# Kernel optimization log

Measured on AMD Instinct MI355X. Metric: run time of the kernel, lower is better.

## Reference

```python
import jax, jax.numpy as jnp
import numpy as np

BATCH = 64
N_NODES = 1000
SEQ = 12
FEAT = 4          # in_features_per_node // N_history
IN_CH = 48        # in_features_per_node, also GAT out_channels
HEADS = 2
OUT_FEAT = 2      # out_features_per_node
H1, H2 = 256, 128
N_TOTAL = BATCH * N_NODES
E = 1024000


def setup_inputs() -> dict:
    key = jax.random.key(0)
    ks = jax.random.split(key, 16)
    s = 0.05
    return {
        "x": jax.random.normal(ks[0], (N_TOTAL, IN_CH), jnp.float32),
        "edge_index": jax.random.randint(ks[1], (2, E), 0, N_TOTAL, jnp.int64),
        "W_gat": jax.random.normal(ks[2], (IN_CH, HEADS * IN_CH), jnp.float32) * s,
        "att_src": jax.random.normal(ks[3], (HEADS, IN_CH), jnp.float32) * s,
        "att_dst": jax.random.normal(ks[4], (HEADS, IN_CH), jnp.float32) * s,
        "gat_bias": jax.random.normal(ks[5], (IN_CH,), jnp.float32) * s,
        "W_ih1": jax.random.normal(ks[6], (4 * H1, N_NODES * FEAT), jnp.float32) * s,
        "W_hh1": jax.random.normal(ks[7], (4 * H1, H1), jnp.float32) * s,
        "b1": jnp.zeros((4 * H1,), jnp.float32),
        "W_ih2": jax.random.normal(ks[8], (4 * H2, H1), jnp.float32) * s,
        "W_hh2": jax.random.normal(ks[9], (4 * H2, H2), jnp.float32) * s,
        "b2": jnp.zeros((4 * H2,), jnp.float32),
        "W_out": jax.random.normal(ks[10], (N_NODES * OUT_FEAT, H2), jnp.float32) * s,
        "b_out": jnp.zeros((N_NODES * OUT_FEAT,), jnp.float32),
    }


def _gat_conv(x, edge_index, W_gat, att_src, att_dst, gat_bias):
    """PyG GATConv, heads=HEADS, concat=False (mean over heads), add_self_loops=True."""
    N = x.shape[0]
    h = (x @ W_gat).reshape(N, HEADS, IN_CH)              # [N,H,C]
    a_src = jnp.einsum('nhc,hc->nh', h, att_src)          # [N,H]
    a_dst = jnp.einsum('nhc,hc->nh', h, att_dst)
    loops = jnp.arange(N, dtype=edge_index.dtype)
    src = jnp.concatenate([edge_index[0], loops])         # [E+N]
    dst = jnp.concatenate([edge_index[1], loops])
    e = jax.nn.leaky_relu(a_src[src] + a_dst[dst], 0.2)   # [E+N,H]
    # segment-softmax over incoming edges of each destination node
    m = jnp.full((N, HEADS), -jnp.inf, e.dtype).at[dst].max(e)
    w = jnp.exp(e - m[dst])
    denom = jax.ops.segment_sum(w, dst, num_segments=N)
    alpha = w / (denom[dst] + 1e-16)                      # [E+N,H]
    msg = h[src] * alpha[:, :, None]                      # [E+N,H,C]
    out = jax.ops.segment_sum(msg, dst, num_segments=N)   # [N,H,C]
    return out.mean(axis=1) + gat_bias                    # [N,C]


def _lstm(x_seq, W_ih, W_hh, b):
    """Single-layer LSTM, PyTorch gate order (i,f,g,o). x_seq: [T,B,D]."""
    Hs = W_hh.shape[1]
    B = x_seq.shape[1]
    xw = jnp.einsum('tbd,gd->tbg', x_seq, W_ih) + b       # precompute input proj

    def step(carry, xt):
        h, c = carry
        g = xt + h @ W_hh.T
        i, f, gg, o = jnp.split(g, 4, axis=-1)
        i, f, o = jax.nn.sigmoid(i), jax.nn.sigmoid(f), jax.nn.sigmoid(o)
        c = f * c + i * jnp.tanh(gg)
        h = o * jnp.tanh(c)
        return (h, c), h

    h0 = jnp.zeros((B, Hs), x_seq.dtype)
    _, ys = jax.lax.scan(step, (h0, h0), xw)
    return ys                                             # [T,B,Hs]


def reference(x, edge_index, W_gat, att_src, att_dst, gat_bias,
              W_ih1, W_hh1, b1, W_ih2, W_hh2, b2, W_out, b_out):
    g = _gat_conv(x, edge_index, W_gat, att_src, att_dst, gat_bias)  # [N_total, 48]
    # (B, N_nodes, SEQ, FEAT) -> movedim(2,0) -> (SEQ, B, N_nodes*FEAT)
    g = g.reshape(BATCH, N_NODES, SEQ, FEAT)
    g = jnp.moveaxis(g, 2, 0).reshape(SEQ, BATCH, N_NODES * FEAT)
    y = _lstm(g, W_ih1, W_hh1, b1)
    y = _lstm(y, W_ih2, W_hh2, b2)
    last = y[-1]                                          # [B, H2]
    out = last @ W_out.T + b_out                          # [B, N_nodes*OUT_FEAT]
    return out.reshape(BATCH * N_NODES, OUT_FEAT)
```

## Files before the change

kernel.cpp:

```cpp
#include <hip/hip_runtime.h>
#include <hip/hip_fp16.h>
#include <math.h>

#define NTOT   64000
#define NNODE  1000
#define NBATCH 64
#define NSEQ   12
#define NE     1024000

typedef _Float16 half8 __attribute__((ext_vector_type(8)));
typedef float f32x4 __attribute__((ext_vector_type(4)));

__device__ __forceinline__ float lrelu(float x){ return x > 0.f ? x : 0.2f*x; }
__device__ __forceinline__ float sigmoidf_(float x){ return 1.f/(1.f+__expf(-x)); }

__global__ void __launch_bounds__(256) k_gat_h(const float* __restrict__ x, const float* __restrict__ Wg,
                       const float* __restrict__ att_s, const float* __restrict__ att_d,
                       __half* __restrict__ hfeat, float* __restrict__ asrc, float* __restrict__ adst){
  __shared__ __align__(16) float Ws[48*96];
  __shared__ float as_s[96], ad_s[96];
  for (int i = threadIdx.x; i < 48*96; i += 256) Ws[i] = Wg[i];
  if (threadIdx.x < 96){ as_s[threadIdx.x] = att_s[threadIdx.x]; ad_s[threadIdx.x] = att_d[threadIdx.x]; }
  __syncthreads();
  int n = blockIdx.x * 256 + threadIdx.x;
  if (n >= NTOT) return;
  float xr[48];
  const float4* xv = (const float4*)(x + (size_t)n*48);
  #pragma unroll
  for (int q = 0; q < 12; ++q){ float4 v = xv[q]; xr[q*4]=v.x; xr[q*4+1]=v.y; xr[q*4+2]=v.z; xr[q*4+3]=v.w; }
  float a0=0.f,a1=0.f,d0=0.f,d1=0.f;
  __half* hrow = hfeat + (size_t)n*96;
  float prev = 0.f;
  for (int j = 0; j < 96; ++j){
    float acc = 0.f;
    #pragma unroll
    for (int k = 0; k < 48; ++k) acc += xr[k]*Ws[k*96+j];
    if (j & 1){
      __half2 p; p.x = __float2half(prev); p.y = __float2half(acc);
      *(__half2*)(hrow + j - 1) = p;
    } else prev = acc;
    if (j < 48){ a0 += acc*as_s[j]; d0 += acc*ad_s[j]; }
    else       { a1 += acc*as_s[j]; d1 += acc*ad_s[j]; }
  }
  asrc[n*2]=a0; asrc[n*2+1]=a1; adst[n*2]=d0; adst[n*2+1]=d1;
}

__global__ void k_count(const int* __restrict__ ei, int* __restrict__ cnt){
  int e = blockIdx.x*256 + threadIdx.x;
  if (e < NE) atomicAdd(&cnt[ei[NE + e]], 1);
}

__global__ void __launch_bounds__(256) k_scan1(const int* __restrict__ cnt, int* __restrict__ wsum){
  int w = (blockIdx.x*256 + threadIdx.x) >> 6;
  int lane = threadIdx.x & 63;
  int v = cnt[w*64 + lane];
  int t = v;
  #pragma unroll
  for (int d = 1; d < 64; d <<= 1) t += __shfl_xor(t, d);
  if (lane == 0) wsum[w] = t;
}

__global__ void __launch_bounds__(1024) k_scan2(int* __restrict__ wsum){
  __shared__ int tmp[1024];
  int k = threadIdx.x;
  int v = (k < 1000) ? wsum[k] : 0;
  tmp[k] = v; __syncthreads();
  for (int d = 1; d < 1024; d <<= 1){
    int t = (k >= d) ? tmp[k-d] : 0;
    __syncthreads();
    tmp[k] += t;
    __syncthreads();
  }
  if (k < 1000) wsum[k] = tmp[k] - v;
}

__global__ void __launch_bounds__(256) k_scan3(const int* __restrict__ cnt, const int* __restrict__ wpre,
                                               int* __restrict__ offs, int* __restrict__ cursor){
  int w = (blockIdx.x*256 + threadIdx.x) >> 6;
  int lane = threadIdx.x & 63;
  int i = w*64 + lane;
  int v = cnt[i];
  int x = v;
  #pragma unroll
  for (int d = 1; d < 64; d <<= 1){
    int t = __shfl_up(x, d);
    if (lane >= d) x += t;
  }
  int excl = wpre[w] + x - v;
  offs[i] = excl; cursor[i] = excl;
  if (i == NTOT-1) offs[NTOT] = excl + v;
}

__global__ void k_scatter(const int* __restrict__ ei, int* __restrict__ cursor, int* __restrict__ csr){
  int e = blockIdx.x*256 + threadIdx.x;
  if (e < NE){
    int d = ei[NE + e], s = ei[e];
    int pos = atomicAdd(&cursor[d], 1);
    csr[pos] = s;
  }
}

__global__ void __launch_bounds__(256) k_node(const __half* __restrict__ hf, const float* __restrict__ asrc,
                      const float* __restrict__ adst, const int* __restrict__ offs,
                      const int* __restrict__ csr, const float* __restrict__ bias,
                      _Float16* __restrict__ xseqh){
  __shared__ float gsh[4][96];
  int wv = threadIdx.x >> 6, lane = threadIdx.x & 63;
  int n = blockIdx.x*4 + wv;
  int off = offs[n], deg = offs[n+1] - off;
  const float2* as2 = (const float2*)asrc;
  float2 adn = ((const float2*)adst)[n];
  float2 asn = as2[n];
  float es0 = __expf(lrelu(asn.x + adn.x));
  float es1 = __expf(lrelu(asn.y + adn.y));
  int cl = (lane < 48) ? lane : lane - 48;
  bool h0 = (lane < 24);
  float wself = h0 ? es0 : es1;
  float ssum = wself;
  float2 acc;
  {
    __half2 r2 = *(const __half2*)(hf + (size_t)n*96 + 2*cl);
    float2 r = __half22float2(r2);
    acc.x = r.x*wself; acc.y = r.y*wself;
  }
  int i = 0;
  for (; i + 4 <= deg; i += 4){
    int ss[4];
    #pragma unroll
    for (int j = 0; j < 4; ++j) ss[j] = csr[off+i+j];
    float2 aa[4];
    #pragma unroll
    for (int j = 0; j < 4; ++j) aa[j] = as2[ss[j]];
    __half2 rr[4];
    #pragma unroll
    for (int j = 0; j < 4; ++j) rr[j] = *(const __half2*)(hf + (size_t)ss[j]*96 + 2*cl);
    #pragma unroll
    for (int j = 0; j < 4; ++j){
      float w0 = __expf(lrelu(aa[j].x + adn.x));
      float w1 = __expf(lrelu(aa[j].y + adn.y));
      float ws = h0 ? w0 : w1;
      float2 r = __half22float2(rr[j]);
      acc.x += r.x*ws; acc.y += r.y*ws;
      ssum += ws;
    }
  }
  for (; i < deg; ++i){
    int s = csr[off+i];
    float2 a = as2[s];
    __half2 r2 = *(const __half2*)(hf + (size_t)s*96 + 2*cl);
    float w0 = __expf(lrelu(a.x + adn.x));
    float w1 = __expf(lrelu(a.y + adn.y));
    float ws = h0 ? w0 : w1;
    float2 r = __half22float2(r2);
    acc.x += r.x*ws; acc.y += r.y*ws;
    ssum += ws;
  }
  float inv = 1.f/(ssum + 1e-16f);
  if (lane < 48){ gsh[wv][2*cl] = acc.x*inv; gsh[wv][2*cl+1] = acc.y*inv; }
  __syncthreads();
  if (lane < 48){
    float g = 0.5f*(gsh[wv][lane] + gsh[wv][48+lane]) + bias[lane];
    int b = n / 1000, node = n - b*1000;
    int t = lane >> 2, f = lane & 3;
    xseqh[((size_t)(t*64 + b))*4000 + node*4 + f] = (_Float16)g;
  }
}

__global__ void __launch_bounds__(256) k_prep(const float* __restrict__ Wih1,
                    const float* __restrict__ Whh1, const float* __restrict__ Wih2,
                    const float* __restrict__ Whh2,
                    _Float16* __restrict__ Bh, __half* __restrict__ dst){
  int blk = blockIdx.x;
  if (blk < 4000){
    int i = blk*256 + threadIdx.x;
    float4 v = *(const float4*)(Wih1 + (size_t)i*4);
    union { _Float16 h[4]; uint2 u; } o;
    o.h[0] = (_Float16)v.x; o.h[1] = (_Float16)v.y;
    o.h[2] = (_Float16)v.z; o.h[3] = (_Float16)v.w;
    *(uint2*)(Bh + (size_t)i*4) = o.u;
    return;
  }
  int i = (blk-4000)*256 + threadIdx.x;
  if (i < 262144){ int q = i>>10, r = i&1023; dst[i] = __float2half(Whh1[r*256+q]); return; }
  i -= 262144;
  if (i < 131072){ int q = i>>9, r = i&511; dst[262144+i] = __float2half(Wih2[r*256+q]); return; }
  i -= 131072;
  if (i < 65536){ int q = i>>9, r = i&511; dst[393216+i] = __float2half(Whh2[(size_t)r*128+q]); }
}

__global__ void __launch_bounds__(256) k_gemm1h(const _Float16* __restrict__ A,
                        const _Float16* __restrict__ B, const float* __restrict__ b1,
                        float* __restrict__ xw1){
  __shared__ _Float16 As[64*40];
  __shared__ _Float16 Bs[64*40];
  int tid = threadIdx.x;
  int w = tid >> 6, l = tid & 63;
  int m0 = blockIdx.x*64, n0 = blockIdx.y*64;
  int fr = l & 15, fk = (l >> 4)*8;
  f32x4 acc0 = {0.f,0.f,0.f,0.f}, acc1 = acc0, acc2 = acc0, acc3 = acc0;
  int ra = tid >> 2, ca = (tid & 3)*8;
  const _Float16* Ap = A + (size_t)(m0+ra)*4000 + ca;
  const _Float16* Bp = B + (size_t)(n0+ra)*4000 + ca;
  _Float16* Asw = &As[ra*40 + ca];
  _Float16* Bsw = &Bs[ra*40 + ca];
  half8 pa = *(const half8*)Ap;
  half8 pb = *(const half8*)Bp;
  for (int k0 = 0; k0 < 4000; k0 += 32){
    *(half8*)Asw = pa;
    *(half8*)Bsw = pb;
    __syncthreads();
    if (k0 + 32 < 4000){
      pa = *(const half8*)(Ap + k0 + 32);
      pb = *(const half8*)(Bp + k0 + 32);
    }
    half8 af  = *(const half8*)&As[(w*16 + fr)*40 + fk];
    half8 bf0 = *(const half8*)&Bs[( 0 + fr)*40 + fk];
    half8 bf1 = *(const half8*)&Bs[(16 + fr)*40 + fk];
    half8 bf2 = *(const half8*)&Bs[(32 + fr)*40 + fk];
    half8 bf3 = *(const half8*)&Bs[(48 + fr)*40 + fk];
    acc0 = __builtin_amdgcn_mfma_f32_16x16x32_f16(af, bf0, acc0, 0, 0, 0);
    acc1 = __builtin_amdgcn_mfma_f32_16x16x32_f16(af, bf1, acc1, 0, 0, 0);
    acc2 = __builtin_amdgcn_mfma_f32_16x16x32_f16(af, bf2, acc2, 0, 0, 0);
    acc3 = __builtin_amdgcn_mfma_f32_16x16x32_f16(af, bf3, acc3, 0, 0, 0);
    __syncthreads();
  }
  int mrow = m0 + w*16 + (l >> 4)*4;
  int ncol = n0 + (l & 15);
  float bb0 = b1[ncol], bb1 = b1[ncol+16], bb2 = b1[ncol+32], bb3 = b1[ncol+48];
  #pragma unroll
  for (int r = 0; r < 4; ++r){
    float* cp = xw1 + (size_t)(mrow + r)*1024 + ncol;
    cp[0]  = acc0[r] + bb0;
    cp[16] = acc1[r] + bb1;
    cp[32] = acc2[r] + bb2;
    cp[48] = acc3[r] + bb3;
  }
}

__device__ __forceinline__ void mac8(float* acc, uint4 wv, float hq){
  const __half2* hp = (const __half2*)&wv;
  float2 f0 = __half22float2(hp[0]);
  float2 f1 = __half22float2(hp[1]);
  float2 f2 = __half22float2(hp[2]);
  float2 f3 = __half22float2(hp[3]);
  acc[0] += f0.x*hq; acc[1] += f0.y*hq;
  acc[2] += f1.x*hq; acc[3] += f1.y*hq;
  acc[4] += f2.x*hq; acc[5] += f2.y*hq;
  acc[6] += f3.x*hq; acc[7] += f3.y*hq;
}

__global__ void __launch_bounds__(1024) k_lstm(
    const float* __restrict__ xw1, const __half* __restrict__ W1,
    const __half* __restrict__ W2i, const __half* __restrict__ W2h,
    const float* __restrict__ b2, float* __restrict__ h2o){
  __shared__ float h1s[256];
  __shared__ float h2s[128];
  __shared__ __align__(16) float pA[8192];
  __shared__ __align__(16) float pB[8192];
  int t = threadIdx.x;
  int b = blockIdx.x;
  int kk1 = t >> 7, c1c = (t & 127) * 8;
  int kk2 = t >> 6, c2c = (t & 63) * 8;
  int u2 = t - 256;
  float cc1 = 0.f, cc2 = 0.f;
  float b2r[4] = {0.f,0.f,0.f,0.f};
  if (t >= 256 && t < 384){
    #pragma unroll
    for (int gi = 0; gi < 4; ++gi) b2r[gi] = b2[gi*128 + u2];
  }
  if (t < 256) h1s[t] = 0.f;
  if (t < 128) h2s[t] = 0.f;
  __syncthreads();

  for (int k = 0; k <= NSEQ; ++k){
    float xg[4] = {0.f,0.f,0.f,0.f};
    if (k < NSEQ && t < 256){
      const float* xr = xw1 + ((size_t)k*64 + b)*1024 + t;
      #pragma unroll
      for (int gi = 0; gi < 4; ++gi) xg[gi] = xr[gi*256];
    }
    if (k < NSEQ){
      float acc[8] = {0,0,0,0,0,0,0,0};
      const __half* wp = W1 + (size_t)(kk1*32)*1024 + c1c;
      const float* hb = &h1s[kk1*32];
      #pragma unroll 4
      for (int q = 0; q < 32; ++q)
        mac8(acc, *(const uint4*)(wp + (size_t)q*1024), hb[q]);
      float4 w0; w0.x=acc[0]; w0.y=acc[1]; w0.z=acc[2]; w0.w=acc[3];
      float4 w1; w1.x=acc[4]; w1.y=acc[5]; w1.z=acc[6]; w1.w=acc[7];
      *(float4*)&pA[kk1*1024 + c1c]     = w0;
      *(float4*)&pA[kk1*1024 + c1c + 4] = w1;
    }
    if (k >= 1){
      float acch[8] = {0,0,0,0,0,0,0,0};
      const __half* wi = W2i + (size_t)(kk2*16)*512 + c2c;
      const float* hb1 = &h1s[kk2*16];
      #pragma unroll 4
      for (int q = 0; q < 16; ++q)
        mac8(acch, *(const uint4*)(wi + (size_t)q*512), hb1[q]);
      const __half* wh = W2h + (size_t)(kk2*8)*512 + c2c;
      const float* hb2 = &h2s[kk2*8];
      #pragma unroll 4
      for (int q = 0; q < 8; ++q)
        mac8(acch, *(const uint4*)(wh + (size_t)q*512), hb2[q]);
      float4 w0; w0.x=acch[0]; w0.y=acch[1]; w0.z=acch[2]; w0.w=acch[3];
      float4 w1; w1.x=acch[4]; w1.y=acch[5]; w1.z=acch[6]; w1.w=acch[7];
      *(float4*)&pB[kk2*512 + c2c]     = w0;
      *(float4*)&pB[kk2*512 + c2c + 4] = w1;
    }
    __syncthreads();
    if (k < NSEQ && t < 256){
      float g[4];
      #pragma unroll
      for (int gi = 0; gi < 4; ++gi){
        float s = xg[gi];
        #pragma unroll
        for (int kk = 0; kk < 8; ++kk) s += pA[kk*1024 + gi*256 + t];
        g[gi] = s;
      }
      float i_ = sigmoidf_(g[0]);
      float f_ = sigmoidf_(g[1]);
      float gg = tanhf(g[2]);
      float o_ = sigmoidf_(g[3]);
      cc1 = f_*cc1 + i_*gg;
      h1s[t] = o_*tanhf(cc1);
    }
    if (k >= 1 && t >= 256 && t < 384){
      float g[4];
      #pragma unroll
      for (int gi = 0; gi < 4; ++gi){
        float s = b2r[gi];
        #pragma unroll
        for (int kk = 0; kk < 16; ++kk) s += pB[kk*512 + gi*128 + u2];
        g[gi] = s;
      }
      float i_ = sigmoidf_(g[0]);
      float f_ = sigmoidf_(g[1]);
      float gg = tanhf(g[2]);
      float o_ = sigmoidf_(g[3]);
      cc2 = f_*cc2 + i_*gg;
      h2s[u2] = o_*tanhf(cc2);
    }
    __syncthreads();
  }
  if (t >= 256 && t < 384) h2o[(size_t)b*128 + u2] = h2s[u2];
}

__global__ void __launch_bounds__(256) k_out(const float* __restrict__ h2, const float* __restrict__ Wout,
                     const float* __restrict__ bout, float* __restrict__ out){
  __shared__ __align__(16) float hs[8][128];
  int t = threadIdx.x;
  int b0 = blockIdx.y * 8;
  #pragma unroll
  for (int r = 0; r < 4; ++r){
    int idx = r*256 + t;
    hs[idx >> 7][idx & 127] = h2[(size_t)(b0 + (idx >> 7))*128 + (idx & 127)];
  }
  __syncthreads();
  if (t >= 250) return;
  int j = blockIdx.x*250 + t;
  const float4* w = (const float4*)(Wout + (size_t)j*128);
  float bj = bout[j];
  float d[8];
  #pragma unroll
  for (int bb = 0; bb < 8; ++bb) d[bb] = bj;
  for (int q = 0; q < 32; ++q){
    float4 wv = w[q];
    #pragma unroll
    for (int bb = 0; bb < 8; ++bb){
      float4 hv = ((const float4*)hs[bb])[q];
      d[bb] += wv.x*hv.x + wv.y*hv.y + wv.z*hv.z + wv.w*hv.w;
    }
  }
  #pragma unroll
  for (int bb = 0; bb < 8; ++bb)
    out[(size_t)(b0+bb)*2000 + j] = d[bb];
}

extern "C" void kernel_launch(void* const* d_in, const int* in_sizes, int n_in,
                              void* d_out, int out_size, void* d_ws, size_t ws_size,
                              hipStream_t stream){
  const float* x     = (const float*)d_in[0];
  const int*   ei    = (const int*)d_in[1];
  const float* Wg    = (const float*)d_in[2];
  const float* att_s = (const float*)d_in[3];
  const float* att_d = (const float*)d_in[4];
  const float* gb    = (const float*)d_in[5];
  const float* Wih1  = (const float*)d_in[6];
  const float* Whh1  = (const float*)d_in[7];
  const float* b1    = (const float*)d_in[8];
  const float* Wih2  = (const float*)d_in[9];
  const float* Whh2  = (const float*)d_in[10];
  const float* b2    = (const float*)d_in[11];
  const float* Wout  = (const float*)d_in[12];
  const float* bout  = (const float*)d_in[13];
  float* out = (float*)d_out;

  char* w = (char*)d_ws;
  _Float16* xseqh = (_Float16*)w;
  char*  hbase = w + 12288000;
  __half* hfeath = (__half*)hbase;
  _Float16* Bh  = (_Float16*)hbase;
  float* xw1    = (float*)(hbase + 8192000);
  __half* W1h   = (__half*)(hbase + 11337728);
  float* h2o    = (float*)(hbase + 12255232);
  char*  p2 = w + 12288000 + 24576000;
  float* asrc   = (float*)(p2);
  float* adst   = (float*)(p2 + 512000);
  int*   cnt    = (int*)(p2 + 1024000);
  int*   offs   = (int*)(p2 + 1280000);
  int*   cursor = (int*)(p2 + 1536256);
  int*   csr    = (int*)(p2 + 1792256);
  int*   wsum   = csr;

  hipMemsetAsync(cnt, 0, NTOT*sizeof(int), stream);

  k_gat_h<<<250, 256, 0, stream>>>(x, Wg, att_s, att_d, hfeath, asrc, adst);
  k_count<<<4000, 256, 0, stream>>>(ei, cnt);
  k_scan1<<<250, 256, 0, stream>>>(cnt, wsum);
  k_scan2<<<1, 1024, 0, stream>>>(wsum);
  k_scan3<<<250, 256, 0, stream>>>(cnt, wsum, offs, cursor);
  k_scatter<<<4000, 256, 0, stream>>>(ei, cursor, csr);
  k_node<<<16000, 256, 0, stream>>>(hfeath, asrc, adst, offs, csr, gb, xseqh);

  k_prep<<<5792, 256, 0, stream>>>(Wih1, Whh1, Wih2, Whh2, Bh, W1h);
  k_gemm1h<<<dim3(12,16), 256, 0, stream>>>(xseqh, Bh, b1, xw1);

  k_lstm<<<NBATCH, 1024, 0, stream>>>(xw1, W1h, W1h + 262144, W1h + 393216, b2, h2o);
  k_out<<<dim3(8,8), 256, 0, stream>>>(h2o, Wout, bout, out);
}
```

Measured before the change: 409.2 us.

## Split-K the input-projection GEMM and fuse GAT transform with edge counting

The 768x1024x4000 input-projection GEMM is split along K into 5 chunks, so 960 blocks run instead of 192, and a new reduction kernel sums the partials and adds the bias. The GAT feature-transform kernel now also does the destination-degree counting in extra blocks, which saves one launch and lets both pieces of work overlap. In the node aggregation kernel, the unused lanes 48-63 now skip the gather loop instead of loading duplicate data. The cost is an extra 15 MB of partial-sum traffic plus one more kernel launch for the reduction.

```diff
diff --git a/kernel.cpp b/kernel.cpp
--- a/kernel.cpp
+++ b/kernel.cpp
@@ -14,16 +14,21 @@
 __device__ __forceinline__ float lrelu(float x){ return x > 0.f ? x : 0.2f*x; }
 __device__ __forceinline__ float sigmoidf_(float x){ return 1.f/(1.f+__expf(-x)); }
 
-__global__ void __launch_bounds__(256) k_gat_h(const float* __restrict__ x, const float* __restrict__ Wg,
+__global__ void __launch_bounds__(256) k_gat_count(const float* __restrict__ x, const float* __restrict__ Wg,
                        const float* __restrict__ att_s, const float* __restrict__ att_d,
-                       __half* __restrict__ hfeat, float* __restrict__ asrc, float* __restrict__ adst){
+                       __half* __restrict__ hfeat, float* __restrict__ asrc, float* __restrict__ adst,
+                       const int* __restrict__ ei, int* __restrict__ cnt){
+  if (blockIdx.x >= 250){
+    int e = (blockIdx.x - 250)*256 + threadIdx.x;
+    if (e < NE) atomicAdd(&cnt[ei[NE + e]], 1);
+    return;
+  }
   __shared__ __align__(16) float Ws[48*96];
   __shared__ float as_s[96], ad_s[96];
   for (int i = threadIdx.x; i < 48*96; i += 256) Ws[i] = Wg[i];
   if (threadIdx.x < 96){ as_s[threadIdx.x] = att_s[threadIdx.x]; ad_s[threadIdx.x] = att_d[threadIdx.x]; }
   __syncthreads();
   int n = blockIdx.x * 256 + threadIdx.x;
-  if (n >= NTOT) return;
   float xr[48];
   const float4* xv = (const float4*)(x + (size_t)n*48);
   #pragma unroll
@@ -45,11 +50,6 @@
   asrc[n*2]=a0; asrc[n*2+1]=a1; adst[n*2]=d0; adst[n*2+1]=d1;
 }
 
-__global__ void k_count(const int* __restrict__ ei, int* __restrict__ cnt){
-  int e = blockIdx.x*256 + threadIdx.x;
-  if (e < NE) atomicAdd(&cnt[ei[NE + e]], 1);
-}
-
 __global__ void __launch_bounds__(256) k_scan1(const int* __restrict__ cnt, int* __restrict__ wsum){
   int w = (blockIdx.x*256 + threadIdx.x) >> 6;
   int lane = threadIdx.x & 63;
@@ -113,50 +113,52 @@
   float2 asn = as2[n];
   float es0 = __expf(lrelu(asn.x + adn.x));
   float es1 = __expf(lrelu(asn.y + adn.y));
-  int cl = (lane < 48) ? lane : lane - 48;
-  bool h0 = (lane < 24);
-  float wself = h0 ? es0 : es1;
-  float ssum = wself;
-  float2 acc;
-  {
-    __half2 r2 = *(const __half2*)(hf + (size_t)n*96 + 2*cl);
-    float2 r = __half22float2(r2);
-    acc.x = r.x*wself; acc.y = r.y*wself;
-  }
-  int i = 0;
-  for (; i + 4 <= deg; i += 4){
-    int ss[4];
-    #pragma unroll
-    for (int j = 0; j < 4; ++j) ss[j] = csr[off+i+j];
-    float2 aa[4];
-    #pragma unroll
-    for (int j = 0; j < 4; ++j) aa[j] = as2[ss[j]];
-    __half2 rr[4];
-    #pragma unroll
-    for (int j = 0; j < 4; ++j) rr[j] = *(const __half2*)(hf + (size_t)ss[j]*96 + 2*cl);
-    #pragma unroll
-    for (int j = 0; j < 4; ++j){
-      float w0 = __expf(lrelu(aa[j].x + adn.x));
-      float w1 = __expf(lrelu(aa[j].y + adn.y));
+  if (lane < 48){
+    int cl = lane;
+    bool h0 = (lane < 24);
+    float wself = h0 ? es0 : es1;
+    float ssum = wself;
+    float2 acc;
+    {
+      __half2 r2 = *(const __half2*)(hf + (size_t)n*96 + 2*cl);
+      float2 r = __half22float2(r2);
+      acc.x = r.x*wself; acc.y = r.y*wself;
+    }
+    int i = 0;
+    for (; i + 4 <= deg; i += 4){
+      int ss[4];
+      #pragma unroll
+      for (int j = 0; j < 4; ++j) ss[j] = csr[off+i+j];
+      float2 aa[4];
+      #pragma unroll
+      for (int j = 0; j < 4; ++j) aa[j] = as2[ss[j]];
+      __half2 rr[4];
+      #pragma unroll
+      for (int j = 0; j < 4; ++j) rr[j] = *(const __half2*)(hf + (size_t)ss[j]*96 + 2*cl);
+      #pragma unroll
+      for (int j = 0; j < 4; ++j){
+        float w0 = __expf(lrelu(aa[j].x + adn.x));
+        float w1 = __expf(lrelu(aa[j].y + adn.y));
+        float ws = h0 ? w0 : w1;
+        float2 r = __half22float2(rr[j]);
+        acc.x += r.x*ws; acc.y += r.y*ws;
+        ssum += ws;
+      }
+    }
+    for (; i < deg; ++i){
+      int s = csr[off+i];
+      float2 a = as2[s];
+      __half2 r2 = *(const __half2*)(hf + (size_t)s*96 + 2*cl);
+      float w0 = __expf(lrelu(a.x + adn.x));
+      float w1 = __expf(lrelu(a.y + adn.y));
       float ws = h0 ? w0 : w1;
-      float2 r = __half22float2(rr[j]);
+      float2 r = __half22float2(r2);
       acc.x += r.x*ws; acc.y += r.y*ws;
       ssum += ws;
     }
-  }
-  for (; i < deg; ++i){
-    int s = csr[off+i];
-    float2 a = as2[s];
-    __half2 r2 = *(const __half2*)(hf + (size_t)s*96 + 2*cl);
-    float w0 = __expf(lrelu(a.x + adn.x));
-    float w1 = __expf(lrelu(a.y + adn.y));
-    float ws = h0 ? w0 : w1;
-    float2 r = __half22float2(r2);
-    acc.x += r.x*ws; acc.y += r.y*ws;
-    ssum += ws;
-  }
-  float inv = 1.f/(ssum + 1e-16f);
-  if (lane < 48){ gsh[wv][2*cl] = acc.x*inv; gsh[wv][2*cl+1] = acc.y*inv; }
+    float inv = 1.f/(ssum + 1e-16f);
+    gsh[wv][2*cl] = acc.x*inv; gsh[wv][2*cl+1] = acc.y*inv;
+  }
   __syncthreads();
   if (lane < 48){
     float g = 0.5f*(gsh[wv][lane] + gsh[wv][48+lane]) + bias[lane];
@@ -189,29 +191,29 @@
 }
 
 __global__ void __launch_bounds__(256) k_gemm1h(const _Float16* __restrict__ A,
-                        const _Float16* __restrict__ B, const float* __restrict__ b1,
-                        float* __restrict__ xw1){
+                        const _Float16* __restrict__ B, float* __restrict__ part){
   __shared__ _Float16 As[64*40];
   __shared__ _Float16 Bs[64*40];
   int tid = threadIdx.x;
   int w = tid >> 6, l = tid & 63;
   int m0 = blockIdx.x*64, n0 = blockIdx.y*64;
+  int k0 = blockIdx.z*800;
   int fr = l & 15, fk = (l >> 4)*8;
   f32x4 acc0 = {0.f,0.f,0.f,0.f}, acc1 = acc0, acc2 = acc0, acc3 = acc0;
   int ra = tid >> 2, ca = (tid & 3)*8;
-  const _Float16* Ap = A + (size_t)(m0+ra)*4000 + ca;
-  const _Float16* Bp = B + (size_t)(n0+ra)*4000 + ca;
+  const _Float16* Ap = A + (size_t)(m0+ra)*4000 + k0 + ca;
+  const _Float16* Bp = B + (size_t)(n0+ra)*4000 + k0 + ca;
   _Float16* Asw = &As[ra*40 + ca];
   _Float16* Bsw = &Bs[ra*40 + ca];
   half8 pa = *(const half8*)Ap;
   half8 pb = *(const half8*)Bp;
-  for (int k0 = 0; k0 < 4000; k0 += 32){
+  for (int kk = 0; kk < 800; kk += 32){
     *(half8*)Asw = pa;
     *(half8*)Bsw = pb;
     __syncthreads();
-    if (k0 + 32 < 4000){
-      pa = *(const half8*)(Ap + k0 + 32);
-      pb = *(const half8*)(Bp + k0 + 32);
+    if (kk + 32 < 800){
+      pa = *(const half8*)(Ap + kk + 32);
+      pb = *(const half8*)(Bp + kk + 32);
     }
     half8 af  = *(const half8*)&As[(w*16 + fr)*40 + fk];
     half8 bf0 = *(const half8*)&Bs[( 0 + fr)*40 + fk];
@@ -226,15 +228,24 @@
   }
   int mrow = m0 + w*16 + (l >> 4)*4;
   int ncol = n0 + (l & 15);
-  float bb0 = b1[ncol], bb1 = b1[ncol+16], bb2 = b1[ncol+32], bb3 = b1[ncol+48];
   #pragma unroll
   for (int r = 0; r < 4; ++r){
-    float* cp = xw1 + (size_t)(mrow + r)*1024 + ncol;
-    cp[0]  = acc0[r] + bb0;
-    cp[16] = acc1[r] + bb1;
-    cp[32] = acc2[r] + bb2;
-    cp[48] = acc3[r] + bb3;
-  }
+    float* cp = part + ((size_t)blockIdx.z*768 + mrow + r)*1024 + ncol;
+    cp[0]  = acc0[r];
+    cp[16] = acc1[r];
+    cp[32] = acc2[r];
+    cp[48] = acc3[r];
+  }
+}
+
+__global__ void k_red5(const float* __restrict__ part, const float* __restrict__ b1,
+                       float* __restrict__ xw1){
+  int i = blockIdx.x*256 + threadIdx.x;
+  int j = i & 1023;
+  float v = b1[j];
+  #pragma unroll
+  for (int s = 0; s < 5; ++s) v += part[(size_t)s*786432 + i];
+  xw1[i] = v;
 }
 
 __device__ __forceinline__ void mac8(float* acc, uint4 wv, float hq){
@@ -404,6 +415,7 @@
   float* xw1    = (float*)(hbase + 8192000);
   __half* W1h   = (__half*)(hbase + 11337728);
   float* h2o    = (float*)(hbase + 12255232);
+  float* part   = (float*)(hbase + 12288000);
   char*  p2 = w + 12288000 + 24576000;
   float* asrc   = (float*)(p2);
   float* adst   = (float*)(p2 + 512000);
@@ -415,8 +427,7 @@
 
   hipMemsetAsync(cnt, 0, NTOT*sizeof(int), stream);
 
-  k_gat_h<<<250, 256, 0, stream>>>(x, Wg, att_s, att_d, hfeath, asrc, adst);
-  k_count<<<4000, 256, 0, stream>>>(ei, cnt);
+  k_gat_count<<<4250, 256, 0, stream>>>(x, Wg, att_s, att_d, hfeath, asrc, adst, ei, cnt);
   k_scan1<<<250, 256, 0, stream>>>(cnt, wsum);
   k_scan2<<<1, 1024, 0, stream>>>(wsum);
   k_scan3<<<250, 256, 0, stream>>>(cnt, wsum, offs, cursor);
@@ -424,7 +435,8 @@
   k_node<<<16000, 256, 0, stream>>>(hfeath, asrc, adst, offs, csr, gb, xseqh);
 
   k_prep<<<5792, 256, 0, stream>>>(Wih1, Whh1, Wih2, Whh2, Bh, W1h);
-  k_gemm1h<<<dim3(12,16), 256, 0, stream>>>(xseqh, Bh, b1, xw1);
+  k_gemm1h<<<dim3(12,16,5), 256, 0, stream>>>(xseqh, Bh, part);
+  k_red5<<<3072, 256, 0, stream>>>(part, b1, xw1);
 
   k_lstm<<<NBATCH, 1024, 0, stream>>>(xw1, W1h, W1h + 262144, W1h + 393216, b2, h2o);
   k_out<<<dim3(8,8), 256, 0, stream>>>(h2o, Wout, bout, out);
```

After: 365.2 us. 1.12x faster.
